# Kernel tuning notes

Measured on AMD Instinct MI355X. Metric: run time of the kernel, lower is better.

The kernel has to match this reference:

```python
import jax, jax.numpy as jnp
import numpy as np

H0, H1, NHID, BATCH = 256, 256, 512, 2048

def setup_inputs() -> dict:
    key = jax.random.key(0)
    k1, k2, k3, k4, k5 = jax.random.split(key, 5)
    initrange = 0.1
    inputs = jax.random.normal(k1, (BATCH, NHID), dtype=jnp.float32)
    labels = jax.random.randint(k2, (BATCH,), 0, H1, dtype=jnp.int32)
    parent_labels = jax.random.randint(k3, (BATCH,), 0, H0, dtype=jnp.int32)
    layer_top_W = jax.random.uniform(k4, (NHID, H0), jnp.float32, -initrange, initrange)
    layer_top_b = jnp.zeros((H0,), jnp.float32)
    layer_bottom_W = jax.random.uniform(k5, (H0, NHID, H1), jnp.float32, -initrange, initrange)
    layer_bottom_b = jnp.zeros((H0, H1), jnp.float32)
    return {"inputs": inputs, "labels": labels, "parent_labels": parent_labels,
            "layer_top_W": layer_top_W, "layer_top_b": layer_top_b,
            "layer_bottom_W": layer_bottom_W, "layer_bottom_b": layer_bottom_b}

def reference(inputs, labels, parent_labels, layer_top_W, layer_top_b,
              layer_bottom_W, layer_bottom_b):
    batch = inputs.shape[0]
    # top-level softmax over coarse classes: [B, H0]
    top_probs = jax.nn.softmax(inputs @ layer_top_W + layer_top_b, axis=1)
    # per-sample gather of expert weight slice [B, NHID, H1] then bmm
    Wb = layer_bottom_W[parent_labels]            # [B, NHID, H1]
    bb = layer_bottom_b[parent_labels]            # [B, H1]
    bottom_logits = jnp.einsum('bd,bdk->bk', inputs, Wb) + bb
    bottom_probs = jax.nn.softmax(bottom_logits, axis=1)
    ar = jnp.arange(batch)
    target_probs = top_probs[ar, parent_labels] * bottom_probs[ar, labels]
    return target_probs
```

## Files before the change

### kernel.cpp

```cpp
#include <hip/hip_runtime.h>

constexpr int BATCH = 2048;
constexpr int NHID  = 512;
constexpr int H0    = 256;
constexpr int H1    = 256;
constexpr int KCH   = 8;
constexpr int DCH   = NHID / KCH;
constexpr int S     = 8;
constexpr int LSTRIDE = 2048;


__global__ __launch_bounds__(256) void k_prep(const int* __restrict__ parents,
                                              int* __restrict__ list,
                                              int* __restrict__ nval) {
    const int p = blockIdx.x, t = threadIdx.x, g = t >> 6, l = t & 63;
    __shared__ int wcnt[4];
    int running = 0;
    for (int c = 0; c < BATCH; c += 256) {
        const bool match = (parents[c + t] == p);
        const unsigned long long mask = __ballot(match);
        if (l == 0) wcnt[g] = __popcll(mask);
        __syncthreads();
        int off = running;
        for (int w = 0; w < g; ++w) off += wcnt[w];
        if (match)
            list[p * LSTRIDE + off + __popcll(mask & ((1ull << l) - 1ull))] = c + t;
        running += wcnt[0] + wcnt[1] + wcnt[2] + wcnt[3];
        __syncthreads();
    }
    if (t == 0) nval[p] = running;
}

__device__ __forceinline__ void chunk_gemv(const float* __restrict__ W,
                                           const float* __restrict__ xw,
                                           int l, float4 acc[S]) {
    for (int d = 0; d < DCH; d += 8) {
        float4 wt[8];
        #pragma unroll
        for (int r = 0; r < 8; ++r)
            wt[r] = *(const float4*)(W + (size_t)(d + r) * 256 + 4 * l);
        #pragma unroll
        for (int r = 0; r < 8; ++r) {
            #pragma unroll
            for (int s = 0; s < S; ++s) {
                const float xv = xw[s * DCH + d + r];
                acc[s].x = fmaf(xv, wt[r].x, acc[s].x);
                acc[s].y = fmaf(xv, wt[r].y, acc[s].y);
                acc[s].z = fmaf(xv, wt[r].z, acc[s].z);
                acc[s].w = fmaf(xv, wt[r].w, acc[s].w);
            }
        }
    }
}

__global__ __launch_bounds__(256) void k_gemv(
    const float* __restrict__ x, const float* __restrict__ topW,
    const float* __restrict__ botW, const int* __restrict__ list,
    const int* __restrict__ nval, float* __restrict__ wstop,
    float* __restrict__ wsbot) {
    const int w = threadIdx.x >> 6, l = threadIdx.x & 63;
    const int u = blockIdx.x * 4 + w;
    __shared__ __align__(16) float xs[4][S][DCH];
    __shared__ int sid[4][S];
    float* xw = &xs[w][0][0];

    if (u < H0 * KCH) {
        const int p = u >> 3, k = u & 7;
        const int n = nval[p];
        const float* W = botW + ((size_t)p * NHID + (size_t)k * DCH) * H1;
        for (int tb = 0; tb < n; tb += S) {
            const int rem = min(S, n - tb);
            if (l < S) sid[w][l] = list[p * LSTRIDE + tb + min(l, rem - 1)];
            #pragma unroll
            for (int i0 = 0; i0 < 2; ++i0) {
                const int i = i0 * 64 + l, s = i >> 4, c = i & 15;
                const int row = list[p * LSTRIDE + tb + min(s, rem - 1)];
                *(float4*)&xs[w][s][4 * c] =
                    *(const float4*)(x + (size_t)row * NHID + k * DCH + 4 * c);
            }
            float4 acc[S];
            #pragma unroll
            for (int s = 0; s < S; ++s) acc[s] = make_float4(0.f, 0.f, 0.f, 0.f);
            chunk_gemv(W, xw, l, acc);
            for (int s = 0; s < rem; ++s)
                *(float4*)(wsbot + ((size_t)sid[w][s] * KCH + k) * H1 + 4 * l) = acc[s];
        }
    } else {
        const int u2 = u - H0 * KCH;
        const int j = u2 >> 3, k = u2 & 7;
        const float* W = topW + (size_t)k * DCH * H0;
        #pragma unroll
        for (int i0 = 0; i0 < 2; ++i0) {
            const int i = i0 * 64 + l, s = i >> 4, c = i & 15;
            *(float4*)&xs[w][s][4 * c] =
                *(const float4*)(x + (size_t)(S * j + s) * NHID + k * DCH + 4 * c);
        }
        float4 acc[S];
        #pragma unroll
        for (int s = 0; s < S; ++s) acc[s] = make_float4(0.f, 0.f, 0.f, 0.f);
        chunk_gemv(W, xw, l, acc);
        #pragma unroll
        for (int s = 0; s < S; ++s)
            *(float4*)(wstop + ((size_t)(S * j + s) * KCH + k) * H0 + 4 * l) = acc[s];
    }
}

__global__ __launch_bounds__(256) void k_fin(
    const int* __restrict__ labels, const int* __restrict__ parents,
    const float* __restrict__ topb, const float* __restrict__ botb,
    const float* __restrict__ wstop, const float* __restrict__ wsbot,
    float* __restrict__ out) {
    const int w = threadIdx.x >> 6, l = threadIdx.x & 63;
    const int s = blockIdx.x * 4 + w;
    const int par = parents[s];
    float pr[2];
    #pragma unroll
    for (int pass = 0; pass < 2; ++pass) {
        const float* wsrc = pass ? wsbot : wstop;
        float4 v = make_float4(0.f, 0.f, 0.f, 0.f);
        #pragma unroll
        for (int k = 0; k < KCH; ++k) {
            const float4 c = *(const float4*)(wsrc + ((size_t)s * KCH + k) * 256 + 4 * l);
            v.x += c.x; v.y += c.y; v.z += c.z; v.w += c.w;
        }
        const float4 bias = pass ? *(const float4*)(botb + (size_t)par * H1 + 4 * l)
                                 : *(const float4*)(topb + 4 * l);
        v.x += bias.x; v.y += bias.y; v.z += bias.z; v.w += bias.w;

        float m = fmaxf(fmaxf(v.x, v.y), fmaxf(v.z, v.w));
        #pragma unroll
        for (int off = 32; off > 0; off >>= 1)
            m = fmaxf(m, __shfl_xor(m, off, 64));

        const float ex = expf(v.x - m), ey = expf(v.y - m);
        const float ez = expf(v.z - m), ew = expf(v.w - m);
        float sum = (ex + ey) + (ez + ew);
        #pragma unroll
        for (int off = 32; off > 0; off >>= 1)
            sum += __shfl_xor(sum, off, 64);

        const int tgt = pass ? labels[s] : par;
        const int c0 = 4 * l;
        float et = (c0 == tgt) ? ex : (c0 + 1 == tgt) ? ey
                 : (c0 + 2 == tgt) ? ez : (c0 + 3 == tgt) ? ew : 0.f;
        #pragma unroll
        for (int off = 32; off > 0; off >>= 1)
            et += __shfl_xor(et, off, 64);

        pr[pass] = et / sum;
    }
    if (l == 0) out[s] = pr[0] * pr[1];
}

extern "C" void kernel_launch(void* const* d_in, const int* in_sizes, int n_in,
                              void* d_out, int out_size, void* d_ws, size_t ws_size,
                              hipStream_t stream) {
    const float* x       = (const float*)d_in[0];
    const int*   labels  = (const int*)  d_in[1];
    const int*   parents = (const int*)  d_in[2];
    const float* topW    = (const float*)d_in[3];
    const float* topb    = (const float*)d_in[4];
    const float* botW    = (const float*)d_in[5];
    const float* botb    = (const float*)d_in[6];
    float*       out     = (float*)d_out;

    int*   list  = (int*)d_ws;
    int*   nval  = (int*)((char*)d_ws + (size_t)H0 * LSTRIDE * sizeof(int));
    float* wstop = (float*)((char*)d_ws + (size_t)H0 * LSTRIDE * sizeof(int) + 4096);
    float* wsbot = wstop + (size_t)BATCH * KCH * H0;

    k_prep<<<H0, 256, 0, stream>>>(parents, list, nval);
    const int units = H0 * KCH + (BATCH / S) * KCH;
    k_gemv<<<units / 4, 256, 0, stream>>>(x, topW, botW, list, nval, wstop, wsbot);
    k_fin<<<BATCH / 4, 256, 0, stream>>>(labels, parents, topb, botb, wstop, wsbot, out);
}
```

Measured before the change: 249.7 us.

## Double-buffer weight loads, halve K-split, and split per-parent batches across slots

Each wave's GEMV now prefetches the next 8 weight rows into a second register buffer while computing on the current ones, so load latency is hidden. The K-split goes from 8 to 4 chunks of 128, and each parent/chunk is served by two waves that take alternating groups of 8 samples. This halves the partial-sum workspace traffic read back in the finalize kernel. In exchange each wave carries more registers (launch_bounds min 2 blocks) and uses more LDS per block. Sample ids now live in registers instead of shared memory. Because two slots share each parent, weight reuse per wave drops and the same weights are read by both waves.

Result: slower. 549.2 us (+119.9%).

```diff
diff --git a/kernel.cpp b/kernel.cpp
--- a/kernel.cpp
+++ b/kernel.cpp
@@ -4,10 +4,13 @@
 constexpr int NHID  = 512;
 constexpr int H0    = 256;
 constexpr int H1    = 256;
-constexpr int KCH   = 8;
+constexpr int KCH   = 4;
 constexpr int DCH   = NHID / KCH;
 constexpr int S     = 8;
+constexpr int NSLOT = 2;
 constexpr int LSTRIDE = 2048;
+constexpr int NBOTW = H0 * KCH * NSLOT;
+constexpr int NTOPW = (BATCH / S) * KCH;
 
 
 __global__ __launch_bounds__(256) void k_prep(const int* __restrict__ parents,
@@ -34,26 +37,52 @@
 __device__ __forceinline__ void chunk_gemv(const float* __restrict__ W,
                                            const float* __restrict__ xw,
                                            int l, float4 acc[S]) {
-    for (int d = 0; d < DCH; d += 8) {
-        float4 wt[8];
-        #pragma unroll
-        for (int r = 0; r < 8; ++r)
-            wt[r] = *(const float4*)(W + (size_t)(d + r) * 256 + 4 * l);
+    float4 bufA[8], bufB[8];
+    #pragma unroll
+    for (int r = 0; r < 8; ++r)
+        bufA[r] = *(const float4*)(W + (size_t)r * 256 + 4 * l);
+    #pragma unroll
+    for (int r = 0; r < 8; ++r)
+        bufB[r] = *(const float4*)(W + (size_t)(8 + r) * 256 + 4 * l);
+
+    #pragma unroll
+    for (int d = 0; d < DCH; d += 16) {
         #pragma unroll
         for (int r = 0; r < 8; ++r) {
             #pragma unroll
             for (int s = 0; s < S; ++s) {
                 const float xv = xw[s * DCH + d + r];
-                acc[s].x = fmaf(xv, wt[r].x, acc[s].x);
-                acc[s].y = fmaf(xv, wt[r].y, acc[s].y);
-                acc[s].z = fmaf(xv, wt[r].z, acc[s].z);
-                acc[s].w = fmaf(xv, wt[r].w, acc[s].w);
+                acc[s].x = fmaf(xv, bufA[r].x, acc[s].x);
+                acc[s].y = fmaf(xv, bufA[r].y, acc[s].y);
+                acc[s].z = fmaf(xv, bufA[r].z, acc[s].z);
+                acc[s].w = fmaf(xv, bufA[r].w, acc[s].w);
             }
         }
-    }
-}
-
-__global__ __launch_bounds__(256) void k_gemv(
+        if (d + 16 < DCH) {
+            #pragma unroll
+            for (int r = 0; r < 8; ++r)
+                bufA[r] = *(const float4*)(W + (size_t)(d + 16 + r) * 256 + 4 * l);
+        }
+        #pragma unroll
+        for (int r = 0; r < 8; ++r) {
+            #pragma unroll
+            for (int s = 0; s < S; ++s) {
+                const float xv = xw[s * DCH + d + 8 + r];
+                acc[s].x = fmaf(xv, bufB[r].x, acc[s].x);
+                acc[s].y = fmaf(xv, bufB[r].y, acc[s].y);
+                acc[s].z = fmaf(xv, bufB[r].z, acc[s].z);
+                acc[s].w = fmaf(xv, bufB[r].w, acc[s].w);
+            }
+        }
+        if (d + 24 < DCH) {
+            #pragma unroll
+            for (int r = 0; r < 8; ++r)
+                bufB[r] = *(const float4*)(W + (size_t)(d + 24 + r) * 256 + 4 * l);
+        }
+    }
+}
+
+__global__ __launch_bounds__(256, 2) void k_gemv(
     const float* __restrict__ x, const float* __restrict__ topW,
     const float* __restrict__ botW, const int* __restrict__ list,
     const int* __restrict__ nval, float* __restrict__ wstop,
@@ -61,37 +90,38 @@
     const int w = threadIdx.x >> 6, l = threadIdx.x & 63;
     const int u = blockIdx.x * 4 + w;
     __shared__ __align__(16) float xs[4][S][DCH];
-    __shared__ int sid[4][S];
     float* xw = &xs[w][0][0];
 
-    if (u < H0 * KCH) {
-        const int p = u >> 3, k = u & 7;
+    if (u < NBOTW) {
+        const int p = u >> 3, k = (u >> 1) & 3, slot = u & 1;
         const int n = nval[p];
         const float* W = botW + ((size_t)p * NHID + (size_t)k * DCH) * H1;
-        for (int tb = 0; tb < n; tb += S) {
+        for (int tb = slot * S; tb < n; tb += NSLOT * S) {
             const int rem = min(S, n - tb);
-            if (l < S) sid[w][l] = list[p * LSTRIDE + tb + min(l, rem - 1)];
-            #pragma unroll
-            for (int i0 = 0; i0 < 2; ++i0) {
-                const int i = i0 * 64 + l, s = i >> 4, c = i & 15;
-                const int row = list[p * LSTRIDE + tb + min(s, rem - 1)];
+            int sid[S];
+            #pragma unroll
+            for (int s = 0; s < S; ++s)
+                sid[s] = list[p * LSTRIDE + tb + min(s, rem - 1)];
+            #pragma unroll
+            for (int i0 = 0; i0 < 4; ++i0) {
+                const int i = i0 * 64 + l, s = i >> 5, c = i & 31;
                 *(float4*)&xs[w][s][4 * c] =
-                    *(const float4*)(x + (size_t)row * NHID + k * DCH + 4 * c);
+                    *(const float4*)(x + (size_t)sid[s] * NHID + k * DCH + 4 * c);
             }
             float4 acc[S];
             #pragma unroll
             for (int s = 0; s < S; ++s) acc[s] = make_float4(0.f, 0.f, 0.f, 0.f);
             chunk_gemv(W, xw, l, acc);
             for (int s = 0; s < rem; ++s)
-                *(float4*)(wsbot + ((size_t)sid[w][s] * KCH + k) * H1 + 4 * l) = acc[s];
+                *(float4*)(wsbot + ((size_t)sid[s] * KCH + k) * H1 + 4 * l) = acc[s];
         }
     } else {
-        const int u2 = u - H0 * KCH;
-        const int j = u2 >> 3, k = u2 & 7;
+        const int u2 = u - NBOTW;
+        const int j = u2 >> 2, k = u2 & 3;
         const float* W = topW + (size_t)k * DCH * H0;
         #pragma unroll
-        for (int i0 = 0; i0 < 2; ++i0) {
-            const int i = i0 * 64 + l, s = i >> 4, c = i & 15;
+        for (int i0 = 0; i0 < 4; ++i0) {
+            const int i = i0 * 64 + l, s = i >> 5, c = i & 31;
             *(float4*)&xs[w][s][4 * c] =
                 *(const float4*)(x + (size_t)(S * j + s) * NHID + k * DCH + 4 * c);
         }
@@ -170,7 +200,8 @@
     float* wsbot = wstop + (size_t)BATCH * KCH * H0;
 
     k_prep<<<H0, 256, 0, stream>>>(parents, list, nval);
-    const int units = H0 * KCH + (BATCH / S) * KCH;
-    k_gemv<<<units / 4, 256, 0, stream>>>(x, topW, botW, list, nval, wstop, wsbot);
-    k_fin<<<BATCH / 4, 256, 0, stream>>>(labels, parents, topb, botb, wstop, wsbot, out);
-}
+    k_gemv<<<(NBOTW + NTOPW) / 4, 256, 0, stream>>>(x, topW, botW, list, nval,
+                                                    wstop, wsbot);
+    k_fin<<<BATCH / 4, 256, 0, stream>>>(labels, parents, topb, botb,
+                                         wstop, wsbot, out);
+}
```
